# Performance work log

Hardware: AMD Instinct MI355X
Metric: run time of the kernel (lower is better)

Reference implementation:

```python
import jax, jax.numpy as jnp
import numpy as np

H = 256        # h_dim
ATTN = 3       # attn_len (structurally fixed: 3 modality pairs / 3 unimodal streams)


def lstm_scan(x, Wih, Whh, b, h0, c0):
    """Standard LSTM (PyTorch gate order i,f,g,o) over time. x: (B,T,D) -> (B,T,H)."""
    def step(carry, xt):
        h, c = carry
        g = xt @ Wih + h @ Whh + b
        i, f, gg, o = jnp.split(g, 4, axis=-1)
        c = jax.nn.sigmoid(f) * c + jax.nn.sigmoid(i) * jnp.tanh(gg)
        h = jax.nn.sigmoid(o) * jnp.tanh(c)
        return (h, c), h
    _, hs = jax.lax.scan(step, (h0, c0), jnp.swapaxes(x, 0, 1))
    return jnp.swapaxes(hs, 0, 1)


def pad_shift(x, shift, padv=0.0):
    """Shift 3D tensor (B,T,D) forward in time by `shift` with constant padding."""
    pad = jnp.full((x.shape[0], shift, x.shape[2]), padv, x.dtype)
    return jnp.concatenate([pad, x[:, :-shift, :]], axis=1)


def setup_inputs() -> dict:
    key = jax.random.key(0)
    ks = jax.random.split(key, 24)
    B, T = 16, 1024
    F, A, Tx = 512, 256, 768
    s = jnp.float32(0.05)
    f32 = jnp.float32
    inp = {
        "x": jax.random.normal(ks[0], (B, T, 1), f32),
        "face_features": jax.random.normal(ks[1], (B, T, F), f32),
        "audio_features": jax.random.normal(ks[2], (B, T, A), f32),
        "text_features": jax.random.normal(ks[3], (B, T, Tx), f32),
        "target": jax.random.normal(ks[4], (B, T, 1), f32),
        "text_W": jax.random.normal(ks[5], (Tx, H), f32) * s,
        "text_b": jnp.zeros((H,), f32),
        "face_W": jax.random.normal(ks[6], (F, H), f32) * s,
        "face_b": jnp.zeros((H,), f32),
        "audio_W": jax.random.normal(ks[7], (A, H), f32) * s,
        "audio_b": jnp.zeros((H,), f32),
        "att_W": jax.random.normal(ks[8], (2 * H,), f32) * s,
        "att_b": jnp.zeros((), f32),
        "ut_W": jax.random.normal(ks[9], (H,), f32) * s,
        "ut_b": jnp.zeros((), f32),
        "uf_W": jax.random.normal(ks[10], (H,), f32) * s,
        "uf_b": jnp.zeros((), f32),
        "ua_W": jax.random.normal(ks[11], (H,), f32) * s,
        "ua_b": jnp.zeros((), f32),
        "enc_Wih": jax.random.normal(ks[12], (ATTN, ATTN, 4 * H), f32) * s,
        "enc_Whh": jax.random.normal(ks[13], (ATTN, H, 4 * H), f32) * s,
        "enc_b": jnp.zeros((ATTN, 4 * H), f32),
        "enc_outW": jax.random.normal(ks[14], (ATTN, H), f32) * s,
        "enc_outb": jnp.zeros((ATTN,), f32),
        "dec_Wih": jax.random.normal(ks[15], (1 + ATTN, 4 * H), f32) * s,
        "dec_Whh": jax.random.normal(ks[16], (H, 4 * H), f32) * s,
        "dec_b": jnp.zeros((4 * H,), f32),
        "dec_h0": jnp.zeros((H,), f32),
        "dec_c0": jnp.zeros((H,), f32),
        "out1_W": jax.random.normal(ks[17], (H, 4), f32) * s,
        "out1_b": jnp.zeros((4,), f32),
        "out2_W": jax.random.normal(ks[18], (4, 1), f32) * s,
        "out2_b": jnp.zeros((1,), f32),
    }
    return inp


def reference(x, face_features, audio_features, text_features, target,
              text_W, text_b, face_W, face_b, audio_W, audio_b,
              att_W, att_b, ut_W, ut_b, uf_W, uf_b, ua_W, ua_b,
              enc_Wih, enc_Whh, enc_b, enc_outW, enc_outb,
              dec_Wih, dec_Whh, dec_b, dec_h0, dec_c0,
              out1_W, out1_b, out2_W, out2_b):
    B, T = x.shape[0], x.shape[1]
    tr = text_features @ text_W + text_b    # (B,T,H)
    fr = face_features @ face_W + face_b
    ar = audio_features @ audio_W + audio_b

    def pair_att(a, b2):  # Linear(2H->1) on tanh(cat), softmax over TIME
        s = jnp.tanh(jnp.concatenate([a, b2], axis=-1)) @ att_W + att_b  # (B,T)
        return jax.nn.softmax(s, axis=-1)

    def uni(rep, W, bb):  # Linear(H->1) on tanh(rep), softmax over TIME
        return jax.nn.softmax(jnp.tanh(rep) @ W + bb, axis=-1)  # (B,T)

    att1 = pair_att(tr, fr); att2 = pair_att(fr, ar); att3 = pair_att(tr, ar)
    enc_input = jnp.concatenate([uni(tr, ut_W, ut_b), uni(fr, uf_W, uf_b),
                                 uni(ar, ua_W, ua_b)], axis=-1).reshape(B, T, ATTN)
    attn = jnp.concatenate([att1, att2, att3], axis=-1).reshape(B, T, ATTN)

    # cLSTM shared encoder: ATTN independent LSTMs over the full 3-dim input,
    # each followed by Linear(H->1); outputs concatenated -> (B,T,ATTN).
    z0 = jnp.zeros((B, H), enc_input.dtype)
    hs = jax.vmap(lambda Wih, Whh, bb: lstm_scan(enc_input, Wih, Whh, bb, z0, z0))(
        enc_Wih, enc_Whh, enc_b)                      # (ATTN,B,T,H)
    enc_out = jnp.einsum('kbth,kh->btk', hs, enc_outW) + enc_outb  # (B,T,ATTN)

    # convolve: local causal weighted sum over ATTN shifted copies
    shifted = jnp.stack([enc_out if i == 0 else pad_shift(enc_out, i)
                         for i in range(ATTN)], axis=-1)           # (B,T,ATTN,ATTN)
    context = jnp.sum(attn[:, :, None, :] * shifted, axis=-1)      # (B,T,ATTN)

    # decoder (teacher forcing path)
    dec_in = jnp.concatenate([pad_shift(target, 1, 0.0), context], axis=2)  # (B,T,1+ATTN)
    dh0 = jnp.tile(dec_h0[None], (B, 1))
    dc0 = jnp.tile(dec_c0[None], (B, 1))
    dec_out = lstm_scan(dec_in, dec_Wih, dec_Whh, dec_b, dh0, dc0)  # (B,T,H)
    predicted = jax.nn.relu(dec_out @ out1_W + out1_b) @ out2_W + out2_b  # (B,T,1)
    return predicted
```

## Files before the change

### kernel.cpp

```cpp
#include <hip/hip_runtime.h>
#include <hip/hip_bf16.h>

typedef float f32x4 __attribute__((ext_vector_type(4)));
typedef __bf16 bf16x8 __attribute__((ext_vector_type(8)));
typedef unsigned long long ull;

#define DEVI static __device__ __forceinline__

DEVI unsigned f2bfu(float f){
  unsigned u = __builtin_bit_cast(unsigned, f);
  return (u + 0x7fffu + ((u >> 16) & 1u)) >> 16;
}
DEVI float bf2f(unsigned s){
  return __builtin_bit_cast(float, s << 16);
}
DEVI float sigf(float x){ return 1.f/(1.f + __expf(-x)); }
DEVI float thf(float x){ return 2.f*sigf(2.f*x) - 1.f; }

__global__ __launch_bounds__(256) void k_pack_lstm(
    const float* __restrict__ encWhh, const float* __restrict__ encWih,
    const float* __restrict__ decWhh, const float* __restrict__ decWih,
    const float* __restrict__ encB,   const float* __restrict__ decB,
    unsigned short* __restrict__ outp)
{
  const int total = 4*16*9*4*64*8;
  for (int e = blockIdx.x*blockDim.x + threadIdx.x; e < total; e += gridDim.x*blockDim.x){
    int j  = e & 7;
    int l  = (e >> 3) & 63;
    int g  = (e >> 9) & 3;
    int r  = e >> 11;
    int kt = r % 9;  r /= 9;
    int w  = r & 15;
    int lstm = r >> 4;
    int k = 32*kt + 8*(l >> 4) + j;
    int n = 256*g + 16*w + (l & 15);
    float v = 0.f;
    if (lstm < 3){
      if (k < 256)       v = encWhh[(lstm*256 + k)*1024 + n];
      else if (k < 259)  v = encWih[(lstm*3 + (k-256))*1024 + n];
      else if (k == 260) v = encB[lstm*1024 + n];
    } else {
      if (k < 256)       v = decWhh[k*1024 + n];
      else if (k < 260)  v = decWih[(k-256)*1024 + n];
      else if (k == 260) v = decB[n];
    }
    outp[e] = (unsigned short)f2bfu(v);
  }
}

__global__ __launch_bounds__(256) void k_pack_B(
    const float* __restrict__ W, int KT, unsigned short* __restrict__ outp)
{
  const int total = 2*KT*8*64*8;
  for (int e = blockIdx.x*blockDim.x + threadIdx.x; e < total; e += gridDim.x*blockDim.x){
    int j  = e & 7;
    int l  = (e >> 3) & 63;
    int nt = (e >> 9) & 7;
    int r  = e >> 12;
    int kt = r % KT;
    int tn = r / KT;
    int k = 32*kt + 8*(l >> 4) + j;
    int n = 128*tn + 16*nt + (l & 15);
    outp[e] = (unsigned short)f2bfu(W[k*256 + n]);
  }
}

__global__ __launch_bounds__(256) void k_proj(
    const float* __restrict__ A, const unsigned short* __restrict__ Bp,
    const float* __restrict__ bias, unsigned short* __restrict__ outT, int K)
{
  __shared__ unsigned char sA[8192];
  __shared__ unsigned char sB[8192];
  const int tid = threadIdx.x;
  const int l = tid & 63;
  const int wv = tid >> 6;
  const int wm = wv >> 1, wn = wv & 1;
  const int tm = blockIdx.x, tn = blockIdx.y;
  const int KT = K >> 5;

  f32x4 acc[4][4];
  #pragma unroll
  for (int a = 0; a < 4; ++a)
    #pragma unroll
    for (int cc = 0; cc < 4; ++cc)
      acc[a][cc] = f32x4{0.f,0.f,0.f,0.f};

  const int arow = tid >> 1;
  const float* Ap = A + (size_t)(tm*128 + arow)*K + (tid & 1)*16;
  const uint4* Bsrc = (const uint4*)Bp + (size_t)tn*KT*512 + tid*2;

  for (int kt = 0; kt < KT; ++kt){
    float4 f0 = *(const float4*)(Ap + kt*32);
    float4 f1 = *(const float4*)(Ap + kt*32 + 4);
    float4 f2 = *(const float4*)(Ap + kt*32 + 8);
    float4 f3 = *(const float4*)(Ap + kt*32 + 12);
    uint4 p0, p1;
    p0.x = f2bfu(f0.x) | (f2bfu(f0.y) << 16);
    p0.y = f2bfu(f0.z) | (f2bfu(f0.w) << 16);
    p0.z = f2bfu(f1.x) | (f2bfu(f1.y) << 16);
    p0.w = f2bfu(f1.z) | (f2bfu(f1.w) << 16);
    p1.x = f2bfu(f2.x) | (f2bfu(f2.y) << 16);
    p1.y = f2bfu(f2.z) | (f2bfu(f2.w) << 16);
    p1.z = f2bfu(f3.x) | (f2bfu(f3.y) << 16);
    p1.w = f2bfu(f3.z) | (f2bfu(f3.w) << 16);
    unsigned base = arow*64 + (tid & 1)*32;
    unsigned sw = (arow & 3) << 4;
    *(uint4*)(sA + ((base)      ^ sw)) = p0;
    *(uint4*)(sA + ((base + 16) ^ sw)) = p1;
    *((uint4*)sB + tid*2)     = Bsrc[kt*512];
    *((uint4*)sB + tid*2 + 1) = Bsrc[kt*512 + 1];
    __syncthreads();

    bf16x8 af[4], bf[4];
    #pragma unroll
    for (int a = 0; a < 4; ++a){
      unsigned row = 64*wm + 16*a + (l & 15);
      unsigned off = (row*64 + 16*(l >> 4)) ^ ((row & 3) << 4);
      af[a] = __builtin_bit_cast(bf16x8, *(const uint4*)(sA + off));
    }
    #pragma unroll
    for (int cc = 0; cc < 4; ++cc){
      unsigned off = ((4*wn + cc)*64 + l)*16;
      bf[cc] = __builtin_bit_cast(bf16x8, *(const uint4*)(sB + off));
    }
    #pragma unroll
    for (int a = 0; a < 4; ++a)
      #pragma unroll
      for (int cc = 0; cc < 4; ++cc)
        acc[a][cc] = __builtin_amdgcn_mfma_f32_16x16x32_bf16(af[a], bf[cc], acc[a][cc], 0, 0, 0);
    __syncthreads();
  }
  #pragma unroll
  for (int cc = 0; cc < 4; ++cc){
    int colg = tn*128 + 64*wn + 16*cc + (l & 15);
    float bs = bias[colg];
    #pragma unroll
    for (int a = 0; a < 4; ++a){
      int rowg = tm*128 + 64*wm + 16*a + 4*(l >> 4);
      #pragma unroll
      for (int r = 0; r < 4; ++r){
        outT[(size_t)(rowg + r)*256 + colg] = (unsigned short)f2bfu(thf(acc[a][cc][r] + bs));
      }
    }
  }
}

__global__ __launch_bounds__(256) void k_attdot(
    const unsigned short* __restrict__ tT, const unsigned short* __restrict__ tF,
    const unsigned short* __restrict__ tA,
    const float* __restrict__ attW, const float* __restrict__ utW,
    const float* __restrict__ ufW, const float* __restrict__ uaW,
    float* __restrict__ s6)
{
  const int l = threadIdx.x & 63;
  const int wid = (blockIdx.x*blockDim.x + threadIdx.x) >> 6;
  const int nw = (gridDim.x*blockDim.x) >> 6;
  float alo[4], ahi[4], wt[4], wf[4], wa[4];
  #pragma unroll
  for (int q = 0; q < 4; ++q){
    alo[q] = attW[4*l + q];
    ahi[q] = attW[256 + 4*l + q];
    wt[q]  = utW[4*l + q];
    wf[q]  = ufW[4*l + q];
    wa[q]  = uaW[4*l + q];
  }
  for (int r = wid; r < 16384; r += nw){
    uint2 vT = *(const uint2*)(tT + (size_t)r*256 + 4*l);
    uint2 vF = *(const uint2*)(tF + (size_t)r*256 + 4*l);
    uint2 vA = *(const uint2*)(tA + (size_t)r*256 + 4*l);
    float xt[4] = { bf2f(vT.x & 0xffff), bf2f(vT.x >> 16), bf2f(vT.y & 0xffff), bf2f(vT.y >> 16) };
    float xf[4] = { bf2f(vF.x & 0xffff), bf2f(vF.x >> 16), bf2f(vF.y & 0xffff), bf2f(vF.y >> 16) };
    float xa[4] = { bf2f(vA.x & 0xffff), bf2f(vA.x >> 16), bf2f(vA.y & 0xffff), bf2f(vA.y >> 16) };
    float ptlo = 0.f, ptu = 0.f, pflo = 0.f, pfhi = 0.f, pfu = 0.f, pahi = 0.f, pau = 0.f;
    #pragma unroll
    for (int q = 0; q < 4; ++q){
      ptlo += xt[q]*alo[q]; ptu += xt[q]*wt[q];
      pflo += xf[q]*alo[q]; pfhi += xf[q]*ahi[q]; pfu += xf[q]*wf[q];
      pahi += xa[q]*ahi[q]; pau += xa[q]*wa[q];
    }
    #pragma unroll
    for (int s = 1; s < 64; s <<= 1){
      ptlo += __shfl_xor(ptlo, s); ptu  += __shfl_xor(ptu, s);
      pflo += __shfl_xor(pflo, s); pfhi += __shfl_xor(pfhi, s);
      pfu  += __shfl_xor(pfu, s);  pahi += __shfl_xor(pahi, s);
      pau  += __shfl_xor(pau, s);
    }
    if (l == 0){
      int o = r;
      s6[o]             = ptlo + pfhi;
      s6[16384 + o]     = pflo + pahi;
      s6[2*16384 + o]   = ptlo + pahi;
      s6[3*16384 + o]   = ptu;
      s6[4*16384 + o]   = pfu;
      s6[5*16384 + o]   = pau;
    }
  }
}

__global__ __launch_bounds__(256) void k_zerofeed(unsigned short* __restrict__ encfeed,
                                                  int* __restrict__ tags)
{
  int i = blockIdx.x*blockDim.x + threadIdx.x;
  if (i < 16384) encfeed[i*4 + 3] = 0;
  if (i < 128) tags[i] = 0;
}

__global__ __launch_bounds__(256) void k_smax(
    const float* __restrict__ s6, float* __restrict__ attn_tb,
    unsigned short* __restrict__ encfeed)
{
  __shared__ float red[4];
  const int f = blockIdx.x >> 4;
  const int b = blockIdx.x & 15;
  const int tid = threadIdx.x;
  const float* row = s6 + f*16384 + b*1024;
  float4 v = *(const float4*)(row + 4*tid);
  float mx = fmaxf(fmaxf(v.x, v.y), fmaxf(v.z, v.w));
  #pragma unroll
  for (int s = 1; s < 64; s <<= 1) mx = fmaxf(mx, __shfl_xor(mx, s));
  if ((tid & 63) == 0) red[tid >> 6] = mx;
  __syncthreads();
  mx = fmaxf(fmaxf(red[0], red[1]), fmaxf(red[2], red[3]));
  float e0 = __expf(v.x - mx), e1 = __expf(v.y - mx), e2 = __expf(v.z - mx), e3 = __expf(v.w - mx);
  float sm = e0 + e1 + e2 + e3;
  __syncthreads();
  #pragma unroll
  for (int s = 1; s < 64; s <<= 1) sm += __shfl_xor(sm, s);
  if ((tid & 63) == 0) red[tid >> 6] = sm;
  __syncthreads();
  sm = red[0] + red[1] + red[2] + red[3];
  float inv = 1.f/sm;
  float e[4] = {e0, e1, e2, e3};
  int ff = (f < 3) ? f : f - 3;
  #pragma unroll
  for (int q = 0; q < 4; ++q){
    int idx = ff*1024 + 4*tid + q;
    int tt = idx/3, kk = idx - 3*tt;
    if (f < 3) attn_tb[(tt*16 + b)*3 + kk] = e[q]*inv;
    else       encfeed[(tt*16 + b)*4 + kk] = (unsigned short)f2bfu(e[q]*inv);
  }
}

__global__ __launch_bounds__(512, 2) void k_lstm(
    const unsigned short* __restrict__ packW,
    const unsigned short* __restrict__ encfeed,
    const float* __restrict__ target,
    const float* __restrict__ attn_tb,
    const float* __restrict__ encOutW,
    const float* __restrict__ encOutB,
    const float* __restrict__ dec_h0,
    const float* __restrict__ dec_c0,
    unsigned short* __restrict__ dec_h,
    ull* __restrict__ exch,
    float* __restrict__ partials,
    int* __restrict__ tags)
{
  __shared__ unsigned char hl[2][16*768];
  __shared__ float ring[3][16][3];
  const int tid = threadIdx.x;
  const int l = tid & 63;
  const int w = tid >> 6;
  const int pair = blockIdx.x >> 1;
  const int half = blockIdx.x & 1;
  const int wglob = half*8 + w;
  const bool isdec = (pair == 3);

  const int b = l & 15;
  const int j0 = 16*wglob + 4*(l >> 4);
  const unsigned swb = (unsigned)(b & 7) << 4;

  float c[4];
  #pragma unroll
  for (int r = 0; r < 4; ++r) c[r] = isdec ? dec_c0[j0 + r] : 0.f;

  float wow[4] = {0.f, 0.f, 0.f, 0.f};
  if (!isdec){
    #pragma unroll
    for (int r = 0; r < 4; ++r) wow[r] = encOutW[pair*256 + j0 + r];
  }

  {
    int ib = tid >> 5;
    int ic = (tid & 31) * 8;
    #pragma unroll
    for (int q = 0; q < 2; ++q){
      int c0 = ic + 4*q;
      uint2 hz;
      if (isdec){
        hz.x = f2bfu(dec_h0[c0])   | (f2bfu(dec_h0[c0+1]) << 16);
        hz.y = f2bfu(dec_h0[c0+2]) | (f2bfu(dec_h0[c0+3]) << 16);
      } else { hz.x = 0u; hz.y = 0u; }
      *(uint2*)(hl[0] + ((ib*768 + 2*c0) ^ ((unsigned)(ib & 7) << 4))) = hz;
    }
  }
  if (tid < 224){
    int bufi = tid / 112;
    int r = tid % 112;
    int bb = r / 7, q = r % 7;
    uint2 z;
    z.x = (q == 0) ? 0x00003f80u : 0u;
    z.y = 0u;
    *(uint2*)(hl[bufi] + ((bb*768 + 520 + 8*q) ^ ((unsigned)(bb & 7) << 4))) = z;
  }
  if (!isdec && tid < 16){
    uint2 gx0 = *(const uint2*)(encfeed + tid*4);
    *(uint2*)(hl[0] + ((tid*768 + 512) ^ ((unsigned)(tid & 7) << 4))) = gx0;
  }

  const uint4* wb = (const uint4*)packW + ((size_t)(pair*16 + wglob)*36)*64 + l;
  uint4 wreg[36];
  #pragma unroll
  for (int i = 0; i < 36; ++i) wreg[i] = wb[i*64];
  #pragma unroll
  for (int i = 0; i < 36; ++i)
    asm volatile("" : "+v"(wreg[i].x), "+v"(wreg[i].y), "+v"(wreg[i].z), "+v"(wreg[i].w));

  int* mytag = tags + (pair*2 + half)*16;
  int* ptag  = tags + (pair*2 + (half^1))*16;

  if (isdec){
    if (tid == 0){
      #pragma unroll
      for (int k = 0; k < 3; ++k)
        #pragma unroll
        for (int h2 = 0; h2 < 2; ++h2)
          while (__hip_atomic_load(tags + (k*2 + h2)*16, __ATOMIC_ACQUIRE, __HIP_MEMORY_SCOPE_AGENT) < 1) {}
    }
    if (tid < 48){
      int bb = tid & 15, kk = tid >> 4;
      ring[1][bb][kk] = 0.f;
      ring[2][bb][kk] = 0.f;
    }
    __syncthreads();
    if (tid < 48){
      int bb = tid & 15, kk = tid >> 4;
      float s = encOutB[kk];
      #pragma unroll
      for (int h2 = 0; h2 < 2; ++h2)
        #pragma unroll
        for (int wv = 0; wv < 8; ++wv)
          s += __hip_atomic_load(partials + (((size_t)0*3 + kk)*2 + h2)*128 + wv*16 + bb,
                                 __ATOMIC_RELAXED, __HIP_MEMORY_SCOPE_AGENT);
      ring[0][bb][kk] = s;
    }
    __syncthreads();
    if (tid < 16){
      int bb = tid;
      float a0 = attn_tb[bb*3 + 0];
      unsigned o0 = 0u;
      unsigned ok[3];
      #pragma unroll
      for (int k = 0; k < 3; ++k) ok[k] = f2bfu(a0 * ring[0][bb][k]);
      uint2 pk; pk.x = o0 | (ok[0] << 16); pk.y = ok[1] | (ok[2] << 16);
      *(uint2*)(hl[0] + ((bb*768 + 512) ^ ((unsigned)(bb & 7) << 4))) = pk;
    }
  }
  __syncthreads();

  for (int t = 0; t < 1024; ++t){
    const int p = t + 1;
    const unsigned char* cur = hl[t & 1];
    unsigned char* nxt = (unsigned char*)hl[p & 1];

    bf16x8 af[9];
    #pragma unroll
    for (int kt = 0; kt < 9; ++kt){
      unsigned off = (unsigned)(b*768 + kt*64 + 16*(l >> 4)) ^ swb;
      af[kt] = __builtin_bit_cast(bf16x8, *(const uint4*)(cur + off));
    }

    uint2 gx;
    const bool ldx = (!isdec) && (t < 1023) && (tid < 16);
    if (ldx) gx = *(const uint2*)(encfeed + (size_t)p*64 + tid*4);

    f32x4 acc[4];
    #pragma unroll
    for (int g = 0; g < 4; ++g) acc[g] = f32x4{0.f,0.f,0.f,0.f};
    #pragma unroll
    for (int kt = 0; kt < 9; ++kt){
      #pragma unroll
      for (int g = 0; g < 4; ++g)
        acc[g] = __builtin_amdgcn_mfma_f32_16x16x32_bf16(
            __builtin_bit_cast(bf16x8, wreg[kt*4 + g]), af[kt], acc[g], 0, 0, 0);
    }

    unsigned hp[4];
    #pragma unroll
    for (int r = 0; r < 4; ++r){
      float vi = sigf(acc[0][r]);
      float vf = sigf(acc[1][r]);
      float vg = thf (acc[2][r]);
      float vo = sigf(acc[3][r]);
      float cc = vf*c[r] + vi*vg;
      c[r] = cc;
      hp[r] = f2bfu(vo * thf(cc));
    }
    uint2 hpk; hpk.x = hp[0] | (hp[1] << 16); hpk.y = hp[2] | (hp[3] << 16);
    *(uint2*)(nxt + ((b*768 + 2*j0) ^ swb)) = hpk;

    if (isdec){
      *(uint2*)(dec_h + (size_t)(t*16 + b)*256 + j0) = hpk;
    } else {
      float s = bf2f(hp[0])*wow[0] + bf2f(hp[1])*wow[1]
              + bf2f(hp[2])*wow[2] + bf2f(hp[3])*wow[3];
      s += __shfl_xor(s, 16);
      s += __shfl_xor(s, 32);
      if (l < 16)
        __hip_atomic_store(partials + (((size_t)t*3 + pair)*2 + half)*128 + w*16 + l,
                           s, __ATOMIC_RELAXED, __HIP_MEMORY_SCOPE_AGENT);
    }

    {
      ull val = ((ull)hpk.y << 32) | (ull)hpk.x;
      int jg = (j0 & 127) >> 2;
      __hip_atomic_store(exch + (((size_t)(pair*2 + (p & 1))*2 + half)*16 + b)*32 + jg,
                         val, __ATOMIC_RELAXED, __HIP_MEMORY_SCOPE_AGENT);
    }
    __syncthreads();
    if (tid == 0){
      __hip_atomic_store(mytag, p, __ATOMIC_RELEASE, __HIP_MEMORY_SCOPE_AGENT);
      while (__hip_atomic_load(ptag, __ATOMIC_ACQUIRE, __HIP_MEMORY_SCOPE_AGENT) < p) {}
      if (isdec && t < 1023){
        #pragma unroll
        for (int k = 0; k < 3; ++k)
          #pragma unroll
          for (int h2 = 0; h2 < 2; ++h2)
            while (__hip_atomic_load(tags + (k*2 + h2)*16, __ATOMIC_ACQUIRE, __HIP_MEMORY_SCOPE_AGENT) < p + 1) {}
      }
    }
    __syncthreads();

    {
      int pb = tid >> 5, pj = tid & 31;
      ull pv = __hip_atomic_load(exch + (((size_t)(pair*2 + (p & 1))*2 + (half^1))*16 + pb)*32 + pj,
                                 __ATOMIC_RELAXED, __HIP_MEMORY_SCOPE_AGENT);
      uint2 pk2; pk2.x = (unsigned)pv; pk2.y = (unsigned)(pv >> 32);
      *(uint2*)(nxt + ((pb*768 + 256*(half^1) + 8*pj) ^ ((unsigned)(pb & 7) << 4))) = pk2;
    }

    if (!isdec){
      if (ldx) *(uint2*)(nxt + ((tid*768 + 512) ^ ((unsigned)(tid & 7) << 4))) = gx;
    } else if (t < 1023){
      if (tid < 48){
        int bb = tid & 15, kk = tid >> 4;
        float s = encOutB[kk];
        #pragma unroll
        for (int h2 = 0; h2 < 2; ++h2)
          #pragma unroll
          for (int wv = 0; wv < 8; ++wv)
            s += __hip_atomic_load(partials + (((size_t)p*3 + kk)*2 + h2)*128 + wv*16 + bb,
                                   __ATOMIC_RELAXED, __HIP_MEMORY_SCOPE_AGENT);
        ring[p % 3][bb][kk] = s;
      }
      __syncthreads();
      if (tid < 16){
        int bb = tid;
        float a0 = attn_tb[((size_t)p*16 + bb)*3 + 0];
        float a1 = attn_tb[((size_t)p*16 + bb)*3 + 1];
        float a2 = attn_tb[((size_t)p*16 + bb)*3 + 2];
        int s0 = p % 3, s1 = (p + 2) % 3, s2 = (p + 1) % 3;
        unsigned o0 = f2bfu(target[bb*1024 + p - 1]);
        unsigned ok[3];
        #pragma unroll
        for (int k = 0; k < 3; ++k)
          ok[k] = f2bfu(a0*ring[s0][bb][k] + a1*ring[s1][bb][k] + a2*ring[s2][bb][k]);
        uint2 pk; pk.x = o0 | (ok[0] << 16); pk.y = ok[1] | (ok[2] << 16);
        *(uint2*)(nxt + ((bb*768 + 512) ^ ((unsigned)(bb & 7) << 4))) = pk;
      }
    }
    __syncthreads();
  }
}

__global__ __launch_bounds__(256) void k_decout(
    const unsigned short* __restrict__ dec_h, const float* __restrict__ W1,
    const float* __restrict__ b1, const float* __restrict__ W2,
    const float* __restrict__ b2, float* __restrict__ out)
{
  const int l = threadIdx.x & 63;
  const int wid = (blockIdx.x*blockDim.x + threadIdx.x) >> 6;
  const int nw = (gridDim.x*blockDim.x) >> 6;
  const int o = l >> 4, jc = l & 15;
  for (int e = wid; e < 16384; e += nw){
    int t = e >> 4, b = e & 15;
    const unsigned short* hr = dec_h + (size_t)(t*16 + b)*256 + jc*16;
    uint4 v0 = *(const uint4*)hr;
    uint4 v1 = *(const uint4*)(hr + 8);
    unsigned vv[8] = {v0.x, v0.y, v0.z, v0.w, v1.x, v1.y, v1.z, v1.w};
    float p = 0.f;
    #pragma unroll
    for (int q = 0; q < 8; ++q){
      int j = jc*16 + 2*q;
      p += bf2f(vv[q] & 0xffff) * W1[j*4 + o];
      p += bf2f(vv[q] >> 16)    * W1[(j + 1)*4 + o];
    }
    p += __shfl_xor(p, 1); p += __shfl_xor(p, 2);
    p += __shfl_xor(p, 4); p += __shfl_xor(p, 8);
    float v = 0.f;
    if (jc == 0) v = fmaxf(p + b1[o], 0.f) * W2[o];
    v += __shfl_xor(v, 16);
    v += __shfl_xor(v, 32);
    if (l == 0) out[b*1024 + t] = v + b2[0];
  }
}

extern "C" void kernel_launch(void* const* d_in, const int* in_sizes, int n_in,
                              void* d_out, int out_size, void* d_ws, size_t ws_size,
                              hipStream_t stream)
{
  const float* faceF   = (const float*)d_in[1];
  const float* audioF  = (const float*)d_in[2];
  const float* textF   = (const float*)d_in[3];
  const float* target  = (const float*)d_in[4];
  const float* textW   = (const float*)d_in[5];
  const float* textB   = (const float*)d_in[6];
  const float* faceW   = (const float*)d_in[7];
  const float* faceB   = (const float*)d_in[8];
  const float* audioW  = (const float*)d_in[9];
  const float* audioB  = (const float*)d_in[10];
  const float* attW    = (const float*)d_in[11];
  const float* utW     = (const float*)d_in[13];
  const float* ufW     = (const float*)d_in[15];
  const float* uaW     = (const float*)d_in[17];
  const float* encWih  = (const float*)d_in[19];
  const float* encWhh  = (const float*)d_in[20];
  const float* encB    = (const float*)d_in[21];
  const float* encOutW = (const float*)d_in[22];
  const float* encOutB = (const float*)d_in[23];
  const float* decWih  = (const float*)d_in[24];
  const float* decWhh  = (const float*)d_in[25];
  const float* decB    = (const float*)d_in[26];
  const float* decH0   = (const float*)d_in[27];
  const float* decC0   = (const float*)d_in[28];
  const float* out1W   = (const float*)d_in[29];
  const float* out1B   = (const float*)d_in[30];
  const float* out2W   = (const float*)d_in[31];
  const float* out2B   = (const float*)d_in[32];
  float* out = (float*)d_out;

  char* ws = (char*)d_ws;
  size_t off = 0;
  auto alloc = [&](size_t bytes) -> void* {
    void* p = ws + off;
    off += (bytes + 255) & ~(size_t)255;
    return p;
  };
  unsigned short* packL   = (unsigned short*)alloc(1179648ull*2);
  unsigned short* packT   = (unsigned short*)alloc(196608ull*2);
  unsigned short* packF   = (unsigned short*)alloc(131072ull*2);
  unsigned short* packA   = (unsigned short*)alloc(65536ull*2);
  unsigned short* tanhT   = (unsigned short*)alloc(16384ull*256*2);
  unsigned short* tanhF   = (unsigned short*)alloc(16384ull*256*2);
  unsigned short* tanhA   = (unsigned short*)alloc(16384ull*256*2);
  float*          s6      = (float*)alloc(6ull*16384*4);
  float*          attn_tb = (float*)alloc(49152ull*4);
  unsigned short* encfeed = (unsigned short*)alloc(65536ull*2);
  unsigned short* dec_h   = (unsigned short*)alloc(1024ull*16*256*2);
  ull*            exch    = (ull*)alloc(8192ull*8);
  float*          partials= (float*)alloc(1024ull*3*2*8*16*4);
  int*            tags    = (int*)alloc(512);
  if (off > ws_size) return;

  hipLaunchKernelGGL(k_pack_lstm, dim3(512), dim3(256), 0, stream,
                     encWhh, encWih, decWhh, decWih, encB, decB, packL);
  hipLaunchKernelGGL(k_pack_B, dim3(256), dim3(256), 0, stream, textW, 24, packT);
  hipLaunchKernelGGL(k_pack_B, dim3(256), dim3(256), 0, stream, faceW, 16, packF);
  hipLaunchKernelGGL(k_pack_B, dim3(128), dim3(256), 0, stream, audioW, 8, packA);

  hipLaunchKernelGGL(k_proj, dim3(128, 2), dim3(256), 0, stream, textF,  packT, textB,  tanhT, 768);
  hipLaunchKernelGGL(k_proj, dim3(128, 2), dim3(256), 0, stream, faceF,  packF, faceB,  tanhF, 512);
  hipLaunchKernelGGL(k_proj, dim3(128, 2), dim3(256), 0, stream, audioF, packA, audioB, tanhA, 256);

  hipLaunchKernelGGL(k_attdot, dim3(256), dim3(256), 0, stream,
                     tanhT, tanhF, tanhA, attW, utW, ufW, uaW, s6);
  hipLaunchKernelGGL(k_zerofeed, dim3(64), dim3(256), 0, stream, encfeed, tags);
  hipLaunchKernelGGL(k_smax, dim3(96), dim3(256), 0, stream, s6, attn_tb, encfeed);

  hipLaunchKernelGGL(k_lstm, dim3(8), dim3(512), 0, stream,
                     packL, encfeed, target, attn_tb, encOutW, encOutB,
                     decH0, decC0, dec_h, exch, partials, tags);
  hipLaunchKernelGGL(k_decout, dim3(256), dim3(256), 0, stream,
                     dec_h, out1W, out1B, out2W, out2B, out);
}
```

Measured before the change: 5.521 ms.

## Replace tag barriers with step-tagged flag-in-data exchange between LSTM block halves

Inter-block synchronization in the recurrent LSTM kernel changes from a release/acquire tag counter plus two block barriers per step to 64-bit words that carry the step number next to the payload. Each thread spins on exactly the hidden-state words and encoder partials it needs, so the tag round trip and one __syncthreads per step go away. Attention and target loads for the decoder are issued early to hide their latency, and the pinned weight registers are constrained to AGPRs. In exchange the exchange and partials buffers double in size and are zeroed by an extra kernel, and correctness now depends on relaxed atomics carrying the tag.

```diff
diff --git a/kernel.cpp b/kernel.cpp
--- a/kernel.cpp
+++ b/kernel.cpp
@@ -16,6 +16,13 @@
 }
 DEVI float sigf(float x){ return 1.f/(1.f + __expf(-x)); }
 DEVI float thf(float x){ return 2.f*sigf(2.f*x) - 1.f; }
+
+DEVI ull allc(const ull* p){
+  return __hip_atomic_load(p, __ATOMIC_RELAXED, __HIP_MEMORY_SCOPE_AGENT);
+}
+DEVI void alst(ull* p, ull v){
+  __hip_atomic_store(p, v, __ATOMIC_RELAXED, __HIP_MEMORY_SCOPE_AGENT);
+}
 
 __global__ __launch_bounds__(256) void k_pack_lstm(
     const float* __restrict__ encWhh, const float* __restrict__ encWih,
@@ -197,12 +204,16 @@
   }
 }
 
-__global__ __launch_bounds__(256) void k_zerofeed(unsigned short* __restrict__ encfeed,
-                                                  int* __restrict__ tags)
+__global__ __launch_bounds__(256) void k_zerofeed(unsigned short* __restrict__ encfeed)
 {
   int i = blockIdx.x*blockDim.x + threadIdx.x;
   if (i < 16384) encfeed[i*4 + 3] = 0;
-  if (i < 128) tags[i] = 0;
+}
+
+__global__ __launch_bounds__(256) void k_zerows(uint4* __restrict__ p, int n)
+{
+  for (int i = blockIdx.x*blockDim.x + threadIdx.x; i < n; i += gridDim.x*blockDim.x)
+    p[i] = uint4{0u,0u,0u,0u};
 }
 
 __global__ __launch_bounds__(256) void k_smax(
@@ -252,11 +263,11 @@
     const float* __restrict__ dec_c0,
     unsigned short* __restrict__ dec_h,
     ull* __restrict__ exch,
-    float* __restrict__ partials,
-    int* __restrict__ tags)
+    ull* __restrict__ partials)
 {
   __shared__ unsigned char hl[2][16*768];
   __shared__ float ring[3][16][3];
+  __shared__ float eo_part[2][48];
   const int tid = threadIdx.x;
   const int l = tid & 63;
   const int w = tid >> 6;
@@ -277,6 +288,11 @@
   if (!isdec){
     #pragma unroll
     for (int r = 0; r < 4; ++r) wow[r] = encOutW[pair*256 + j0 + r];
+  }
+  float eb[3] = {0.f, 0.f, 0.f};
+  if (isdec && tid < 16){
+    #pragma unroll
+    for (int k = 0; k < 3; ++k) eb[k] = encOutB[k];
   }
 
   {
@@ -312,46 +328,43 @@
   #pragma unroll
   for (int i = 0; i < 36; ++i) wreg[i] = wb[i*64];
   #pragma unroll
-  for (int i = 0; i < 36; ++i)
-    asm volatile("" : "+v"(wreg[i].x), "+v"(wreg[i].y), "+v"(wreg[i].z), "+v"(wreg[i].w));
-
-  int* mytag = tags + (pair*2 + half)*16;
-  int* ptag  = tags + (pair*2 + (half^1))*16;
+  for (int i = 0; i < 36; ++i){
+    unsigned t0 = wreg[i].x, t1 = wreg[i].y, t2 = wreg[i].z, t3 = wreg[i].w;
+    asm volatile("" : "+a"(t0), "+a"(t1), "+a"(t2), "+a"(t3));
+    wreg[i].x = t0; wreg[i].y = t1; wreg[i].z = t2; wreg[i].w = t3;
+  }
 
   if (isdec){
-    if (tid == 0){
+    if (tid < 96){
+      int bb = tid & 15, kk = (tid >> 4) % 3, h2 = tid / 48;
+      const ull* p8 = partials + (((size_t)0*3 + kk)*2 + h2)*128 + bb;
+      ull v[8];
       #pragma unroll
-      for (int k = 0; k < 3; ++k)
-        #pragma unroll
-        for (int h2 = 0; h2 < 2; ++h2)
-          while (__hip_atomic_load(tags + (k*2 + h2)*16, __ATOMIC_ACQUIRE, __HIP_MEMORY_SCOPE_AGENT) < 1) {}
-    }
-    if (tid < 48){
-      int bb = tid & 15, kk = tid >> 4;
-      ring[1][bb][kk] = 0.f;
-      ring[2][bb][kk] = 0.f;
-    }
-    __syncthreads();
-    if (tid < 48){
-      int bb = tid & 15, kk = tid >> 4;
-      float s = encOutB[kk];
-      #pragma unroll
-      for (int h2 = 0; h2 < 2; ++h2)
+      for (int wv = 0; wv < 8; ++wv) v[wv] = allc(p8 + wv*16);
+      bool ok = false;
+      while (!ok){
+        ok = true;
         #pragma unroll
         for (int wv = 0; wv < 8; ++wv)
-          s += __hip_atomic_load(partials + (((size_t)0*3 + kk)*2 + h2)*128 + wv*16 + bb,
-                                 __ATOMIC_RELAXED, __HIP_MEMORY_SCOPE_AGENT);
-      ring[0][bb][kk] = s;
+          if ((unsigned)(v[wv] >> 32) != 1u){ v[wv] = allc(p8 + wv*16); ok = false; }
+      }
+      float s = 0.f;
+      #pragma unroll
+      for (int wv = 0; wv < 8; ++wv) s += __builtin_bit_cast(float, (unsigned)v[wv]);
+      eo_part[h2][kk*16 + bb] = s;
     }
     __syncthreads();
     if (tid < 16){
       int bb = tid;
       float a0 = attn_tb[bb*3 + 0];
-      unsigned o0 = 0u;
-      unsigned ok[3];
+      unsigned ok3[3];
       #pragma unroll
-      for (int k = 0; k < 3; ++k) ok[k] = f2bfu(a0 * ring[0][bb][k]);
-      uint2 pk; pk.x = o0 | (ok[0] << 16); pk.y = ok[1] | (ok[2] << 16);
+      for (int k = 0; k < 3; ++k){
+        float eo = eb[k] + eo_part[0][k*16 + bb] + eo_part[1][k*16 + bb];
+        ring[0][bb][k] = eo; ring[1][bb][k] = 0.f; ring[2][bb][k] = 0.f;
+        ok3[k] = f2bfu(a0*eo);
+      }
+      uint2 pk; pk.x = (ok3[0] << 16); pk.y = ok3[1] | (ok3[2] << 16);
       *(uint2*)(hl[0] + ((bb*768 + 512) ^ ((unsigned)(bb & 7) << 4))) = pk;
     }
   }
@@ -372,6 +385,14 @@
     uint2 gx;
     const bool ldx = (!isdec) && (t < 1023) && (tid < 16);
     if (ldx) gx = *(const uint2*)(encfeed + (size_t)p*64 + tid*4);
+    float at0 = 0.f, at1 = 0.f, at2 = 0.f, tg = 0.f;
+    const bool bld = isdec && (t < 1023) && (tid < 16);
+    if (bld){
+      at0 = attn_tb[((size_t)p*16 + tid)*3 + 0];
+      at1 = attn_tb[((size_t)p*16 + tid)*3 + 1];
+      at2 = attn_tb[((size_t)p*16 + tid)*3 + 2];
+      tg  = target[tid*1024 + t];
+    }
 
     f32x4 acc[4];
     #pragma unroll
@@ -406,69 +427,66 @@
       s += __shfl_xor(s, 16);
       s += __shfl_xor(s, 32);
       if (l < 16)
-        __hip_atomic_store(partials + (((size_t)t*3 + pair)*2 + half)*128 + w*16 + l,
-                           s, __ATOMIC_RELAXED, __HIP_MEMORY_SCOPE_AGENT);
-    }
-
-    {
-      ull val = ((ull)hpk.y << 32) | (ull)hpk.x;
-      int jg = (j0 & 127) >> 2;
-      __hip_atomic_store(exch + (((size_t)(pair*2 + (p & 1))*2 + half)*16 + b)*32 + jg,
-                         val, __ATOMIC_RELAXED, __HIP_MEMORY_SCOPE_AGENT);
-    }
-    __syncthreads();
-    if (tid == 0){
-      __hip_atomic_store(mytag, p, __ATOMIC_RELEASE, __HIP_MEMORY_SCOPE_AGENT);
-      while (__hip_atomic_load(ptag, __ATOMIC_ACQUIRE, __HIP_MEMORY_SCOPE_AGENT) < p) {}
-      if (isdec && t < 1023){
+        alst(partials + (((size_t)t*3 + pair)*2 + half)*128 + w*16 + l,
+             ((ull)(unsigned)p << 32) | (ull)__builtin_bit_cast(unsigned, s));
+    }
+
+    if (t < 1023){
+      {
+        size_t xs = ((((size_t)pair*2 + (p & 1))*2 + half)*16 + b)*64
+                  + ((unsigned)(j0 & 127) >> 1);
+        alst(exch + xs,     ((ull)(unsigned)p << 32) | (ull)hpk.x);
+        alst(exch + xs + 1, ((ull)(unsigned)p << 32) | (ull)hpk.y);
+      }
+      const int pb2 = tid >> 5, pj = tid & 31;
+      const ull* rb = exch + ((((size_t)pair*2 + (p & 1))*2 + (half^1))*16 + pb2)*64 + pj*2;
+      ull v0 = allc(rb), v1 = allc(rb + 1);
+      const bool pol = isdec && (tid < 96);
+      const int kk = (tid >> 4) % 3, h2 = tid / 48, bb = tid & 15;
+      const ull* p8 = partials + (((size_t)p*3 + kk)*2 + h2)*128 + bb;
+      ull pv[8];
+      if (pol){
         #pragma unroll
-        for (int k = 0; k < 3; ++k)
-          #pragma unroll
-          for (int h2 = 0; h2 < 2; ++h2)
-            while (__hip_atomic_load(tags + (k*2 + h2)*16, __ATOMIC_ACQUIRE, __HIP_MEMORY_SCOPE_AGENT) < p + 1) {}
-      }
-    }
-    __syncthreads();
-
-    {
-      int pb = tid >> 5, pj = tid & 31;
-      ull pv = __hip_atomic_load(exch + (((size_t)(pair*2 + (p & 1))*2 + (half^1))*16 + pb)*32 + pj,
-                                 __ATOMIC_RELAXED, __HIP_MEMORY_SCOPE_AGENT);
-      uint2 pk2; pk2.x = (unsigned)pv; pk2.y = (unsigned)(pv >> 32);
-      *(uint2*)(nxt + ((pb*768 + 256*(half^1) + 8*pj) ^ ((unsigned)(pb & 7) << 4))) = pk2;
-    }
-
-    if (!isdec){
-      if (ldx) *(uint2*)(nxt + ((tid*768 + 512) ^ ((unsigned)(tid & 7) << 4))) = gx;
-    } else if (t < 1023){
-      if (tid < 48){
-        int bb = tid & 15, kk = tid >> 4;
-        float s = encOutB[kk];
-        #pragma unroll
-        for (int h2 = 0; h2 < 2; ++h2)
+        for (int wv = 0; wv < 8; ++wv) pv[wv] = allc(p8 + wv*16);
+      }
+      while (((unsigned)(v0 >> 32) != (unsigned)p) || ((unsigned)(v1 >> 32) != (unsigned)p)){
+        if ((unsigned)(v0 >> 32) != (unsigned)p) v0 = allc(rb);
+        if ((unsigned)(v1 >> 32) != (unsigned)p) v1 = allc(rb + 1);
+      }
+      uint2 pk2; pk2.x = (unsigned)v0; pk2.y = (unsigned)v1;
+      *(uint2*)(nxt + ((pb2*768 + 256*(half^1) + 8*pj) ^ ((unsigned)(pb2 & 7) << 4))) = pk2;
+      if (pol){
+        const unsigned want = (unsigned)(p + 1);
+        bool ok = false;
+        while (!ok){
+          ok = true;
           #pragma unroll
           for (int wv = 0; wv < 8; ++wv)
-            s += __hip_atomic_load(partials + (((size_t)p*3 + kk)*2 + h2)*128 + wv*16 + bb,
-                                   __ATOMIC_RELAXED, __HIP_MEMORY_SCOPE_AGENT);
-        ring[p % 3][bb][kk] = s;
-      }
+            if ((unsigned)(pv[wv] >> 32) != want){ pv[wv] = allc(p8 + wv*16); ok = false; }
+        }
+        float s2 = 0.f;
+        #pragma unroll
+        for (int wv = 0; wv < 8; ++wv) s2 += __builtin_bit_cast(float, (unsigned)pv[wv]);
+        eo_part[h2][kk*16 + bb] = s2;
+      }
+      if (ldx) *(uint2*)(nxt + ((tid*768 + 512) ^ ((unsigned)(tid & 7) << 4))) = gx;
       __syncthreads();
-      if (tid < 16){
-        int bb = tid;
-        float a0 = attn_tb[((size_t)p*16 + bb)*3 + 0];
-        float a1 = attn_tb[((size_t)p*16 + bb)*3 + 1];
-        float a2 = attn_tb[((size_t)p*16 + bb)*3 + 2];
-        int s0 = p % 3, s1 = (p + 2) % 3, s2 = (p + 1) % 3;
-        unsigned o0 = f2bfu(target[bb*1024 + p - 1]);
-        unsigned ok[3];
-        #pragma unroll
-        for (int k = 0; k < 3; ++k)
-          ok[k] = f2bfu(a0*ring[s0][bb][k] + a1*ring[s1][bb][k] + a2*ring[s2][bb][k]);
-        uint2 pk; pk.x = o0 | (ok[0] << 16); pk.y = ok[1] | (ok[2] << 16);
-        *(uint2*)(nxt + ((bb*768 + 512) ^ ((unsigned)(bb & 7) << 4))) = pk;
-      }
-    }
-    __syncthreads();
+      if (isdec){
+        if (tid < 16){
+          int s0 = p % 3, s1 = (p + 2) % 3, s2i = (p + 1) % 3;
+          unsigned ok3[3];
+          #pragma unroll
+          for (int k = 0; k < 3; ++k){
+            float eo = eb[k] + eo_part[0][k*16 + tid] + eo_part[1][k*16 + tid];
+            ring[s0][tid][k] = eo;
+            ok3[k] = f2bfu(at0*eo + at1*ring[s1][tid][k] + at2*ring[s2i][tid][k]);
+          }
+          uint2 pk3; pk3.x = f2bfu(tg) | (ok3[0] << 16); pk3.y = ok3[1] | (ok3[2] << 16);
+          *(uint2*)(nxt + ((tid*768 + 512) ^ ((unsigned)(tid & 7) << 4))) = pk3;
+        }
+        __syncthreads();
+      }
+    }
   }
 }
 
@@ -556,9 +574,8 @@
   float*          attn_tb = (float*)alloc(49152ull*4);
   unsigned short* encfeed = (unsigned short*)alloc(65536ull*2);
   unsigned short* dec_h   = (unsigned short*)alloc(1024ull*16*256*2);
-  ull*            exch    = (ull*)alloc(8192ull*8);
-  float*          partials= (float*)alloc(1024ull*3*2*8*16*4);
-  int*            tags    = (int*)alloc(512);
+  ull*            exch    = (ull*)alloc(16384ull*8);
+  ull*            partials= (ull*)alloc(786432ull*8);
   if (off > ws_size) return;
 
   hipLaunchKernelGGL(k_pack_lstm, dim3(512), dim3(256), 0, stream,
@@ -566,6 +583,8 @@
   hipLaunchKernelGGL(k_pack_B, dim3(256), dim3(256), 0, stream, textW, 24, packT);
   hipLaunchKernelGGL(k_pack_B, dim3(256), dim3(256), 0, stream, faceW, 16, packF);
   hipLaunchKernelGGL(k_pack_B, dim3(128), dim3(256), 0, stream, audioW, 8, packA);
+  hipLaunchKernelGGL(k_zerows, dim3(1024), dim3(256), 0, stream,
+                     (uint4*)exch, (int)((16384ull*8 + 786432ull*8) / 16));
 
   hipLaunchKernelGGL(k_proj, dim3(128, 2), dim3(256), 0, stream, textF,  packT, textB,  tanhT, 768);
   hipLaunchKernelGGL(k_proj, dim3(128, 2), dim3(256), 0, stream, faceF,  packF, faceB,  tanhF, 512);
@@ -573,12 +592,12 @@
 
   hipLaunchKernelGGL(k_attdot, dim3(256), dim3(256), 0, stream,
                      tanhT, tanhF, tanhA, attW, utW, ufW, uaW, s6);
-  hipLaunchKernelGGL(k_zerofeed, dim3(64), dim3(256), 0, stream, encfeed, tags);
+  hipLaunchKernelGGL(k_zerofeed, dim3(64), dim3(256), 0, stream, encfeed);
   hipLaunchKernelGGL(k_smax, dim3(96), dim3(256), 0, stream, s6, attn_tb, encfeed);
 
   hipLaunchKernelGGL(k_lstm, dim3(8), dim3(512), 0, stream,
                      packL, encfeed, target, attn_tb, encOutW, encOutB,
-                     decH0, decC0, dec_h, exch, partials, tags);
+                     decH0, decC0, dec_h, exch, partials);
   hipLaunchKernelGGL(k_decout, dim3(256), dim3(256), 0, stream,
                      dec_h, out1W, out1B, out2W, out2B, out);
 }
```

Measured after the change: 4.852 ms. -12.1%, faster.
